# Kernel tuning notes

Measured on AMD Instinct MI355X. Metric: run time of the kernel, lower is better.

## Reference

```python
import jax, jax.numpy as jnp
import numpy as np

B, L, K, W, DIM, HEADS, DH = 8, 8, 32, 8, 256, 8, 32  # dim = heads*dim_head


def setup_inputs() -> dict:
    key = jax.random.key(0)
    ks = jax.random.split(key, 8)
    rn = lambda k, sh: jax.random.normal(k, sh, dtype=jnp.float32)
    return {
        "ego_feats": rn(ks[0], (B, K, DIM, W, W)),
        "other_feats": rn(ks[1], (B, L, K, DIM, W, W)),
        "W_qkv_ego": rn(ks[2], (DIM, 3 * HEADS * DH)) * 0.02,
        "W_qkv_other": rn(ks[3], (DIM, 3 * HEADS * DH)) * 0.02,
        "W_out_ego": rn(ks[4], (DIM, DIM)) * 0.02,
        "b_out_ego": jnp.zeros((DIM,), jnp.float32),
        "W_out_other": rn(ks[5], (DIM, DIM)) * 0.02,
        "b_out_other": jnp.zeros((DIM,), jnp.float32),
    }


def _qkv(x, Wqkv):
    # x: [b, l, k, w, w, C] -> q/k/v each [b, m, k, n=(w*w), l, c]
    b, l, k, w1, w2, _ = x.shape
    t = (x @ Wqkv).reshape(b, l, k, w1 * w2, 3, HEADS, DH)
    t = jnp.moveaxis(t, 4, 0)                  # [3, b, l, k, n, m, c]
    t = jnp.transpose(t, (0, 1, 5, 3, 4, 2, 6))  # [3, b, m, k, n, l, c]
    return t[0], t[1], t[2]


def reference(ego_feats, other_feats, W_qkv_ego, W_qkv_other,
              W_out_ego, b_out_ego, W_out_other, b_out_other):
    w = ego_feats.shape[-1]
    scale = DH ** -0.5
    # ego: [B,k,C,w,w] -> [B,1,k,w,w,C];  others: [B,L,k,C,w,w] -> [B,L,k,w,w,C]
    x_e = jnp.transpose(ego_feats, (0, 1, 3, 4, 2))[:, None]
    x_o = jnp.transpose(other_feats, (0, 1, 2, 4, 5, 3))
    q_e, k_e, v_e = _qkv(x_e, W_qkv_ego)
    q_o, k_o, v_o = _qkv(x_o, W_qkv_other)
    # per-window, per-pixel cross attention over the agent axis (i,j)
    a_e = jax.nn.softmax(jnp.einsum('bmknic,bmknjc->bmknij', q_e, k_o) * scale, axis=-1)
    a_o = jax.nn.softmax(jnp.einsum('bmknic,bmknjc->bmknij', q_o, k_e) * scale, axis=-1)
    o_e = jnp.einsum('bmknij,bmknjc->bmknic', a_e, v_o)  # [b,m,k,n,1,c]
    o_o = jnp.einsum('bmknij,bmknjc->bmknic', a_o, v_e)  # [b,m,k,n,L,c]

    def merge(t):
        # [b,m,k,n,l,c] -> [b,l,k,w,w,m*c]
        bb, m, kk, n, l, cc = t.shape
        return jnp.transpose(t, (0, 4, 2, 3, 1, 5)).reshape(bb, l, kk, w, w, m * cc)

    out_e = merge(o_e) @ W_out_ego + b_out_ego
    out_o = merge(o_o) @ W_out_other + b_out_other
    out_e = jnp.transpose(out_e, (0, 1, 2, 5, 3, 4))[:, 0]  # [B,k,C,w,w]
    out_o = jnp.transpose(out_o, (0, 1, 2, 5, 3, 4))        # [B,L,k,C,w,w]
    return out_e, out_o
```

## Files before the change

kernel.cpp:

```cpp
#include <hip/hip_runtime.h>


typedef unsigned short u16;
typedef u16  u16x8 __attribute__((ext_vector_type(8)));
typedef u16  u16x4 __attribute__((ext_vector_type(4)));
typedef __bf16 bf16x8 __attribute__((ext_vector_type(8)));
typedef float f32x4 __attribute__((ext_vector_type(4)));

#define XS   264
#define QS   272
#define YSF  68

__device__ __forceinline__ u16 f2bf(float f) {
  union { float f; unsigned u; } t; t.f = f;
  unsigned r = t.u + 0x7FFF + ((t.u >> 16) & 1);
  return (u16)(r >> 16);
}
__device__ __forceinline__ float bf2f(u16 x) {
  union { unsigned u; float f; } t; t.u = ((unsigned)x) << 16;
  return t.f;
}

template <int MT>
__device__ __forceinline__ void gemm_run(const u16* __restrict__ WT,
                                         const u16* __restrict__ X,
                                         int wave, int col, int quad,
                                         f32x4 (&acc)[MT][4]) {
#pragma unroll
  for (int mt = 0; mt < MT; ++mt)
#pragma unroll
    for (int nt = 0; nt < 4; ++nt)
      acc[mt][nt] = (f32x4)(0.0f);
  for (int ks = 0; ks < 8; ++ks) {
    bf16x8 bfr[4];
#pragma unroll
    for (int nt = 0; nt < 4; ++nt)
      bfr[nt] = __builtin_bit_cast(
          bf16x8, *(const u16x8*)&X[(nt * 16 + col) * XS + ks * 32 + quad * 8]);
#pragma unroll
    for (int mt = 0; mt < MT; ++mt) {
      const int m = (wave * MT + mt) * 16 + col;
      bf16x8 afr = __builtin_bit_cast(
          bf16x8, *(const u16x8*)&WT[m * 256 + ks * 32 + quad * 8]);
#pragma unroll
      for (int nt = 0; nt < 4; ++nt)
        acc[mt][nt] = __builtin_amdgcn_mfma_f32_16x16x32_bf16(
            afr, bfr[nt], acc[mt][nt], 0, 0, 0);
    }
  }
}

__global__ void ca_setup_fuse(const float* __restrict__ Wqkv_e,
                              const float* __restrict__ Woo,
                              u16* __restrict__ WCQ) {
  const int c = blockIdx.x, o = threadIdx.x;
  __shared__ float wv[256];
  wv[o] = Wqkv_e[c * 768 + 512 + o];
  __syncthreads();
  float s = 0.f;
#pragma unroll 8
  for (int j = 0; j < 256; ++j) s += wv[j] * Woo[j * 256 + o];
  WCQ[o * 256 + c] = f2bf(s);
}

__global__ void ca_setup_trans(const float* __restrict__ Wqkv_e,
                               const float* __restrict__ Wqkv_o,
                               const float* __restrict__ Woe,
                               u16* __restrict__ WCQ, u16* __restrict__ WKV,
                               u16* __restrict__ WOET) {
  const int bid = blockIdx.x;
  const int job = bid >> 4, ot = (bid >> 2) & 3, ct = bid & 3;
  const float* src; int stride, coff; u16* dst;
  if (job == 0)      { src = Wqkv_e; stride = 768; coff = 0;   dst = WCQ + 65536; }
  else if (job == 1) { src = Wqkv_o; stride = 768; coff = 256; dst = WKV; }
  else if (job == 2) { src = Wqkv_o; stride = 768; coff = 512; dst = WKV + 65536; }
  else               { src = Woe;    stride = 256; coff = 0;   dst = WOET; }
  __shared__ float tile[64][65];
  const int t = threadIdx.x, tc = t & 15, tr = t >> 4;
#pragma unroll
  for (int j = 0; j < 4; ++j) {
    const int cl = tr + j * 16;
    const f32x4 v =
        *(const f32x4*)&src[(ct * 64 + cl) * stride + coff + ot * 64 + tc * 4];
#pragma unroll
    for (int e = 0; e < 4; ++e) tile[cl][tc * 4 + e] = v[e];
  }
  __syncthreads();
#pragma unroll
  for (int j = 0; j < 4; ++j) {
    const int ol = tr + j * 16;
    u16x4 p;
#pragma unroll
    for (int e = 0; e < 4; ++e) p[e] = f2bf(tile[tc * 4 + e][ol]);
    *(u16x4*)&dst[(ot * 64 + ol) * 256 + ct * 64 + tc * 4] = p;
  }
}

__device__ __forceinline__ void tile_load(const float* __restrict__ src, int t,
                                          f32x4 (&g)[2][4]) {
#pragma unroll
  for (int it = 0; it < 2; ++it) {
    const int id = t + it * 512;
    const int n0 = (id & 15) * 4, c0 = (id >> 4) * 4;
#pragma unroll
    for (int i = 0; i < 4; ++i)
      g[it][i] = __builtin_nontemporal_load(
          (const f32x4*)&src[(c0 + i) * 64 + n0]);
  }
}
__device__ __forceinline__ void tile_write(const f32x4 (&g)[2][4],
                                           u16* __restrict__ xbuf, int t) {
#pragma unroll
  for (int it = 0; it < 2; ++it) {
    const int id = t + it * 512;
    const int n0 = (id & 15) * 4, c0 = (id >> 4) * 4;
#pragma unroll
    for (int n = 0; n < 4; ++n) {
      u16x4 p;
#pragma unroll
      for (int i = 0; i < 4; ++i) p[i] = f2bf(g[it][i][n]);
      *(u16x4*)&xbuf[(n0 + n) * XS + c0] = p;
    }
  }
}

__device__ __forceinline__ void agent_step(
    const f32x4 (&gcur)[2][4], f32x4 (&gnxt)[2][4], int Lnxt, bool do_pf,
    const float* __restrict__ xo_base, u16* __restrict__ xbuf,
    u16* __restrict__ kvbuf, const u16* __restrict__ WKV,
    const u16x8 (&qp)[4], float (&oacc)[32], float& m_run, float& s_run,
    int t, int wave, int col, int quad, int an, int ah) {
  tile_write(gcur, xbuf, t);
  __syncthreads();
  if (do_pf) tile_load(xo_base + (size_t)Lnxt * 524288, t, gnxt);

  f32x4 acc[2][4];
  gemm_run<2>(WKV, xbuf, wave, col, quad, acc);
#pragma unroll
  for (int mt = 0; mt < 2; ++mt) {
    const int ob = (wave * 2 + mt) * 16 + quad * 4;
#pragma unroll
    for (int nt = 0; nt < 4; ++nt) {
      u16x4 pk;
#pragma unroll
      for (int r = 0; r < 4; ++r) pk[r] = f2bf(acc[mt][nt][r]);
      *(u16x4*)&kvbuf[(nt * 16 + col) * XS + ob] = pk;
    }
  }
  __syncthreads();

  u16x8 ck[4];
#pragma unroll
  for (int jj = 0; jj < 4; ++jj)
    ck[jj] = *(const u16x8*)&kvbuf[an * XS + ah * 32 + jj * 8];
  __syncthreads();

  float sc = 0.f;
#pragma unroll
  for (int jj = 0; jj < 4; ++jj)
#pragma unroll
    for (int e = 0; e < 8; ++e) sc += bf2f(qp[jj][e]) * bf2f(ck[jj][e]);
  sc *= 0.17677669529663687f;

  gemm_run<2>(WKV + 65536, xbuf, wave, col, quad, acc);
#pragma unroll
  for (int mt = 0; mt < 2; ++mt) {
    const int ob = (wave * 2 + mt) * 16 + quad * 4;
#pragma unroll
    for (int nt = 0; nt < 4; ++nt) {
      u16x4 pv;
#pragma unroll
      for (int r = 0; r < 4; ++r) pv[r] = f2bf(acc[mt][nt][r]);
      *(u16x4*)&kvbuf[(nt * 16 + col) * XS + ob] = pv;
    }
  }
  const float mnew = fmaxf(m_run, sc);
  const float p = __expf(sc - mnew);
  const float al = __expf(m_run - mnew);
  s_run = s_run * al + p;
  m_run = mnew;
  __syncthreads();

  u16x8 cv[4];
#pragma unroll
  for (int jj = 0; jj < 4; ++jj)
    cv[jj] = *(const u16x8*)&kvbuf[an * XS + ah * 32 + jj * 8];
#pragma unroll
  for (int jj = 0; jj < 4; ++jj)
#pragma unroll
    for (int e = 0; e < 8; ++e)
      oacc[jj * 8 + e] = oacc[jj * 8 + e] * al + p * bf2f(cv[jj][e]);
}

__global__ __launch_bounds__(512, 2) void ca_fused(
    const float* __restrict__ ego, const float* __restrict__ other,
    const float* __restrict__ b_oo, const float* __restrict__ b_oe,
    const u16* __restrict__ WCQ, const u16* __restrict__ WKV,
    const u16* __restrict__ WOET, float* __restrict__ out) {
  const int g = blockIdx.x;
  const int bk = (g & 7) * 32 + (g >> 3);
  const int b = bk >> 5, kk = bk & 31;
  const int t = threadIdx.x;
  const int lane = t & 63, wave = t >> 6;
  const int col = lane & 15, quad = lane >> 4;
  const int an = t & 63, ah = t >> 6;

  __shared__ u16 xbuf[64 * XS];
  __shared__ u16 kvbuf[64 * XS];
  __shared__ __align__(16) char ubuf[64 * QS * 2];
  u16*   qbuf = (u16*)ubuf;
  float* ybuf = (float*)ubuf;

  const float* xe_src  = ego + (size_t)bk * 16384;
  const float* xo_base = other + (size_t)(b * 256 + kk) * 16384;
  float* outO = out + 4194304;

  f32x4 gA[2][4], gB[2][4];
  tile_load(xe_src, t, gA);
  tile_write(gA, xbuf, t);
  __syncthreads();
  tile_load(xo_base, t, gB);

  f32x4 accY[2][4], accQ[2][4];
  gemm_run<2>(WCQ, xbuf, wave, col, quad, accY);
  gemm_run<2>(WCQ + 65536, xbuf, wave, col, quad, accQ);
#pragma unroll
  for (int mt = 0; mt < 2; ++mt) {
    const int ob = (wave * 2 + mt) * 16 + quad * 4;
#pragma unroll
    for (int nt = 0; nt < 4; ++nt) {
      u16x4 pq;
#pragma unroll
      for (int r = 0; r < 4; ++r) pq[r] = f2bf(accQ[mt][nt][r]);
      *(u16x4*)&qbuf[(nt * 16 + col) * QS + ob] = pq;
    }
  }
  __syncthreads();

  u16x8 qp[4];
#pragma unroll
  for (int jj = 0; jj < 4; ++jj)
    qp[jj] = *(const u16x8*)&qbuf[an * QS + ah * 32 + jj * 8];
  __syncthreads();

  const int n4 = (t & 15) * 4, cb = t >> 4;
  const size_t obase = (size_t)(b * 256 + kk) * 16384;

  if (wave < 4) {
#pragma unroll
    for (int mt = 0; mt < 2; ++mt)
#pragma unroll
      for (int nt = 0; nt < 4; ++nt)
#pragma unroll
        for (int r = 0; r < 4; ++r)
          ybuf[(wave * 32 + mt * 16 + quad * 4 + r) * YSF + nt * 16 + col] =
              accY[mt][nt][r];
  }
  __syncthreads();
#pragma unroll
  for (int it = 0; it < 4; ++it) {
    const int C = cb + it * 32;
    f32x4 v = *(const f32x4*)&ybuf[C * YSF + n4];
    const float bias = b_oo[C];
#pragma unroll
    for (int e = 0; e < 4; ++e) v[e] += bias;
#pragma unroll
    for (int l = 0; l < 8; ++l)
      __builtin_nontemporal_store(
          v, (f32x4*)&outO[obase + (size_t)l * 524288 + C * 64 + n4]);
  }
  __syncthreads();
  if (wave >= 4) {
#pragma unroll
    for (int mt = 0; mt < 2; ++mt)
#pragma unroll
      for (int nt = 0; nt < 4; ++nt)
#pragma unroll
        for (int r = 0; r < 4; ++r)
          ybuf[((wave - 4) * 32 + mt * 16 + quad * 4 + r) * YSF + nt * 16 + col] =
              accY[mt][nt][r];
  }
  __syncthreads();
#pragma unroll
  for (int it = 0; it < 4; ++it) {
    const int C = 128 + cb + it * 32;
    f32x4 v = *(const f32x4*)&ybuf[(C - 128) * YSF + n4];
    const float bias = b_oo[C];
#pragma unroll
    for (int e = 0; e < 4; ++e) v[e] += bias;
#pragma unroll
    for (int l = 0; l < 8; ++l)
      __builtin_nontemporal_store(
          v, (f32x4*)&outO[obase + (size_t)l * 524288 + C * 64 + n4]);
  }
  __syncthreads();

  float m_run = -3.0e38f, s_run = 0.f;
  float oacc[32];
#pragma unroll
  for (int c = 0; c < 32; ++c) oacc[c] = 0.f;

#pragma unroll 1
  for (int l = 0; l < 8; l += 2) {
    agent_step(gB, gA, l + 1, true, xo_base, xbuf, kvbuf, WKV,
               qp, oacc, m_run, s_run, t, wave, col, quad, an, ah);
    agent_step(gA, gB, l + 2, (l + 2 < 8), xo_base, xbuf, kvbuf, WKV,
               qp, oacc, m_run, s_run, t, wave, col, quad, an, ah);
  }

  {
    const float inv = 1.f / s_run;
#pragma unroll
    for (int jj = 0; jj < 4; ++jj) {
      u16x8 pa;
#pragma unroll
      for (int e = 0; e < 8; ++e) pa[e] = f2bf(oacc[jj * 8 + e] * inv);
      *(u16x8*)&xbuf[an * XS + ah * 32 + jj * 8] = pa;
    }
  }
  __syncthreads();

  f32x4 accE[2][4];
  gemm_run<2>(WOET, xbuf, wave, col, quad, accE);
  if (wave < 4) {
#pragma unroll
    for (int mt = 0; mt < 2; ++mt)
#pragma unroll
      for (int nt = 0; nt < 4; ++nt)
#pragma unroll
        for (int r = 0; r < 4; ++r)
          ybuf[(wave * 32 + mt * 16 + quad * 4 + r) * YSF + nt * 16 + col] =
              accE[mt][nt][r];
  }
  __syncthreads();
#pragma unroll
  for (int it = 0; it < 4; ++it) {
    const int C = cb + it * 32;
    f32x4 v = *(const f32x4*)&ybuf[C * YSF + n4];
    const float bias = b_oe[C];
#pragma unroll
    for (int e = 0; e < 4; ++e) v[e] += bias;
    *(f32x4*)&out[((size_t)(bk * 256 + C)) * 64 + n4] = v;
  }
  __syncthreads();
  if (wave >= 4) {
#pragma unroll
    for (int mt = 0; mt < 2; ++mt)
#pragma unroll
      for (int nt = 0; nt < 4; ++nt)
#pragma unroll
        for (int r = 0; r < 4; ++r)
          ybuf[((wave - 4) * 32 + mt * 16 + quad * 4 + r) * YSF + nt * 16 + col] =
              accE[mt][nt][r];
  }
  __syncthreads();
#pragma unroll
  for (int it = 0; it < 4; ++it) {
    const int C = 128 + cb + it * 32;
    f32x4 v = *(const f32x4*)&ybuf[(C - 128) * YSF + n4];
    const float bias = b_oe[C];
#pragma unroll
    for (int e = 0; e < 4; ++e) v[e] += bias;
    *(f32x4*)&out[((size_t)(bk * 256 + C)) * 64 + n4] = v;
  }
}

extern "C" void kernel_launch(void* const* d_in, const int* in_sizes, int n_in,
                              void* d_out, int out_size, void* d_ws,
                              size_t ws_size, hipStream_t stream) {
  const float* ego    = (const float*)d_in[0];
  const float* other  = (const float*)d_in[1];
  const float* Wqkv_e = (const float*)d_in[2];
  const float* Wqkv_o = (const float*)d_in[3];
  const float* Woe    = (const float*)d_in[4];
  const float* boe    = (const float*)d_in[5];
  const float* Woo    = (const float*)d_in[6];
  const float* boo    = (const float*)d_in[7];
  float* out = (float*)d_out;

  u16* WCQ  = (u16*)d_ws;
  u16* WKV  = WCQ + 512 * 256;
  u16* WOET = WKV + 512 * 256;

  ca_setup_fuse<<<256, 256, 0, stream>>>(Wqkv_e, Woo, WCQ);
  ca_setup_trans<<<64, 256, 0, stream>>>(Wqkv_e, Wqkv_o, Woe, WCQ, WKV, WOET);
  ca_fused<<<256, 512, 0, stream>>>(ego, other, boo, boe, WCQ, WKV, WOET, out);
}
```

Before: 384.0 us.

## Double-buffer agent tiles in LDS and spread broadcast output stores across loop

```diff
diff --git a/kernel.cpp b/kernel.cpp
--- a/kernel.cpp
+++ b/kernel.cpp
@@ -8,6 +8,7 @@
 typedef float f32x4 __attribute__((ext_vector_type(4)));
 
 #define XS   264
+#define KVS  280
 #define QS   272
 #define YSF  68
 
@@ -125,17 +126,23 @@
 }
 
 __device__ __forceinline__ void agent_step(
-    const f32x4 (&gcur)[2][4], f32x4 (&gnxt)[2][4], int Lnxt, bool do_pf,
-    const float* __restrict__ xo_base, u16* __restrict__ xbuf,
+    int L, bool pf, const float* __restrict__ xo_base,
+    const u16* __restrict__ xc, u16* __restrict__ xn,
     u16* __restrict__ kvbuf, const u16* __restrict__ WKV,
+    float* __restrict__ outO, size_t obase, const f32x4 (&yreg)[8],
     const u16x8 (&qp)[4], float (&oacc)[32], float& m_run, float& s_run,
-    int t, int wave, int col, int quad, int an, int ah) {
-  tile_write(gcur, xbuf, t);
-  __syncthreads();
-  if (do_pf) tile_load(xo_base + (size_t)Lnxt * 524288, t, gnxt);
+    int t, int wave, int col, int quad, int an, int ah, int n4, int cb) {
+  f32x4 g[2][4];
+  if (pf) tile_load(xo_base + (size_t)(L + 1) * 524288, t, g);
+
+#pragma unroll
+  for (int it = 0; it < 8; ++it) {
+    const int C = cb + it * 32;
+    *(f32x4*)&outO[obase + (size_t)L * 524288 + C * 64 + n4] = yreg[it];
+  }
 
   f32x4 acc[2][4];
-  gemm_run<2>(WKV, xbuf, wave, col, quad, acc);
+  gemm_run<2>(WKV, xc, wave, col, quad, acc);
 #pragma unroll
   for (int mt = 0; mt < 2; ++mt) {
     const int ob = (wave * 2 + mt) * 16 + quad * 4;
@@ -144,7 +151,7 @@
       u16x4 pk;
 #pragma unroll
       for (int r = 0; r < 4; ++r) pk[r] = f2bf(acc[mt][nt][r]);
-      *(u16x4*)&kvbuf[(nt * 16 + col) * XS + ob] = pk;
+      *(u16x4*)&kvbuf[(nt * 16 + col) * KVS + ob] = pk;
     }
   }
   __syncthreads();
@@ -152,7 +159,7 @@
   u16x8 ck[4];
 #pragma unroll
   for (int jj = 0; jj < 4; ++jj)
-    ck[jj] = *(const u16x8*)&kvbuf[an * XS + ah * 32 + jj * 8];
+    ck[jj] = *(const u16x8*)&kvbuf[an * KVS + ah * 32 + jj * 8];
   __syncthreads();
 
   float sc = 0.f;
@@ -162,7 +169,7 @@
     for (int e = 0; e < 8; ++e) sc += bf2f(qp[jj][e]) * bf2f(ck[jj][e]);
   sc *= 0.17677669529663687f;
 
-  gemm_run<2>(WKV + 65536, xbuf, wave, col, quad, acc);
+  gemm_run<2>(WKV + 65536, xc, wave, col, quad, acc);
 #pragma unroll
   for (int mt = 0; mt < 2; ++mt) {
     const int ob = (wave * 2 + mt) * 16 + quad * 4;
@@ -171,9 +178,11 @@
       u16x4 pv;
 #pragma unroll
       for (int r = 0; r < 4; ++r) pv[r] = f2bf(acc[mt][nt][r]);
-      *(u16x4*)&kvbuf[(nt * 16 + col) * XS + ob] = pv;
-    }
-  }
+      *(u16x4*)&kvbuf[(nt * 16 + col) * KVS + ob] = pv;
+    }
+  }
+  if (pf) tile_write(g, xn, t);
+
   const float mnew = fmaxf(m_run, sc);
   const float p = __expf(sc - mnew);
   const float al = __expf(m_run - mnew);
@@ -184,12 +193,13 @@
   u16x8 cv[4];
 #pragma unroll
   for (int jj = 0; jj < 4; ++jj)
-    cv[jj] = *(const u16x8*)&kvbuf[an * XS + ah * 32 + jj * 8];
+    cv[jj] = *(const u16x8*)&kvbuf[an * KVS + ah * 32 + jj * 8];
 #pragma unroll
   for (int jj = 0; jj < 4; ++jj)
 #pragma unroll
     for (int e = 0; e < 8; ++e)
       oacc[jj * 8 + e] = oacc[jj * 8 + e] * al + p * bf2f(cv[jj][e]);
+  __syncthreads();
 }
 
 __global__ __launch_bounds__(512, 2) void ca_fused(
@@ -204,9 +214,11 @@
   const int lane = t & 63, wave = t >> 6;
   const int col = lane & 15, quad = lane >> 4;
   const int an = t & 63, ah = t >> 6;
-
-  __shared__ u16 xbuf[64 * XS];
-  __shared__ u16 kvbuf[64 * XS];
+  const int n4 = (t & 15) * 4, cb = t >> 4;
+
+  __shared__ u16 x0[64 * XS];
+  __shared__ u16 x1[64 * XS];
+  __shared__ u16 kvbuf[64 * KVS];
   __shared__ __align__(16) char ubuf[64 * QS * 2];
   u16*   qbuf = (u16*)ubuf;
   float* ybuf = (float*)ubuf;
@@ -214,16 +226,21 @@
   const float* xe_src  = ego + (size_t)bk * 16384;
   const float* xo_base = other + (size_t)(b * 256 + kk) * 16384;
   float* outO = out + 4194304;
-
-  f32x4 gA[2][4], gB[2][4];
-  tile_load(xe_src, t, gA);
-  tile_write(gA, xbuf, t);
-  __syncthreads();
-  tile_load(xo_base, t, gB);
+  const size_t obase = (size_t)(b * 256 + kk) * 16384;
+
+  {
+    f32x4 ge[2][4];
+    tile_load(xe_src, t, ge);
+    tile_write(ge, x0, t);
+  }
+  __syncthreads();
+
+  f32x4 g0[2][4];
+  tile_load(xo_base, t, g0);
 
   f32x4 accY[2][4], accQ[2][4];
-  gemm_run<2>(WCQ, xbuf, wave, col, quad, accY);
-  gemm_run<2>(WCQ + 65536, xbuf, wave, col, quad, accQ);
+  gemm_run<2>(WCQ, x0, wave, col, quad, accY);
+  gemm_run<2>(WCQ + 65536, x0, wave, col, quad, accQ);
 #pragma unroll
   for (int mt = 0; mt < 2; ++mt) {
     const int ob = (wave * 2 + mt) * 16 + quad * 4;
@@ -241,11 +258,10 @@
 #pragma unroll
   for (int jj = 0; jj < 4; ++jj)
     qp[jj] = *(const u16x8*)&qbuf[an * QS + ah * 32 + jj * 8];
-  __syncthreads();
-
-  const int n4 = (t & 15) * 4, cb = t >> 4;
-  const size_t obase = (size_t)(b * 256 + kk) * 16384;
-
+  tile_write(g0, x0, t);
+  __syncthreads();
+
+  f32x4 yreg[8];
   if (wave < 4) {
 #pragma unroll
     for (int mt = 0; mt < 2; ++mt)
@@ -264,10 +280,7 @@
     const float bias = b_oo[C];
 #pragma unroll
     for (int e = 0; e < 4; ++e) v[e] += bias;
-#pragma unroll
-    for (int l = 0; l < 8; ++l)
-      __builtin_nontemporal_store(
-          v, (f32x4*)&outO[obase + (size_t)l * 524288 + C * 64 + n4]);
+    yreg[it] = v;
   }
   __syncthreads();
   if (wave >= 4) {
@@ -288,10 +301,7 @@
     const float bias = b_oo[C];
 #pragma unroll
     for (int e = 0; e < 4; ++e) v[e] += bias;
-#pragma unroll
-    for (int l = 0; l < 8; ++l)
-      __builtin_nontemporal_store(
-          v, (f32x4*)&outO[obase + (size_t)l * 524288 + C * 64 + n4]);
+    yreg[4 + it] = v;
   }
   __syncthreads();
 
@@ -302,10 +312,12 @@
 
 #pragma unroll 1
   for (int l = 0; l < 8; l += 2) {
-    agent_step(gB, gA, l + 1, true, xo_base, xbuf, kvbuf, WKV,
-               qp, oacc, m_run, s_run, t, wave, col, quad, an, ah);
-    agent_step(gA, gB, l + 2, (l + 2 < 8), xo_base, xbuf, kvbuf, WKV,
-               qp, oacc, m_run, s_run, t, wave, col, quad, an, ah);
+    agent_step(l, true, xo_base, x0, x1, kvbuf, WKV, outO, obase,
+               yreg, qp, oacc, m_run, s_run,
+               t, wave, col, quad, an, ah, n4, cb);
+    agent_step(l + 1, l + 1 < 7, xo_base, x1, x0, kvbuf, WKV, outO, obase,
+               yreg, qp, oacc, m_run, s_run,
+               t, wave, col, quad, an, ah, n4, cb);
   }
 
   {
@@ -315,13 +327,13 @@
       u16x8 pa;
 #pragma unroll
       for (int e = 0; e < 8; ++e) pa[e] = f2bf(oacc[jj * 8 + e] * inv);
-      *(u16x8*)&xbuf[an * XS + ah * 32 + jj * 8] = pa;
+      *(u16x8*)&x0[an * XS + ah * 32 + jj * 8] = pa;
     }
   }
   __syncthreads();
 
   f32x4 accE[2][4];
-  gemm_run<2>(WOET, xbuf, wave, col, quad, accE);
+  gemm_run<2>(WOET, x0, wave, col, quad, accE);
   if (wave < 4) {
 #pragma unroll
     for (int mt = 0; mt < 2; ++mt)
```

Result: no change. 384.0 us (-0.0%).
